# Performance work log

Measured on AMD Instinct MI355X. Metric: run time of the kernel, lower is better.

Reference implementation:

```python
import jax, jax.numpy as jnp
from jax import lax
import numpy as np

B, S, MEL = 64, 1024, 60
H, L = 180, 4
FS = 3          # mel_smooth_filter_size (num shifted conv branches)
BLOCKS = 3      # mel_smooth_layers
G = MEL // FS   # 20 output units per grouped conv
POST, OUT = 8192, 300


def setup_inputs() -> dict:
    key = jax.random.key(0)
    ks = jax.random.split(key, 13)
    rn = lambda k, shape, s: jax.random.normal(k, shape, jnp.float32) * s
    x = jax.random.normal(ks[0], (B, S, MEL), jnp.float32)
    lens = jax.random.randint(ks[1], (B,), 1, S + 1)
    conv_w = rn(ks[2], (BLOCKS, FS, G, FS, 5), 0.2)   # per block, per shift: (O=20, I/g=3, k=5)
    conv_b = rn(ks[3], (BLOCKS, FS, G), 0.1)
    lstm_wih0 = rn(ks[4], (4 * H, MEL), 0.08)
    lstm_wih_rest = rn(ks[5], (L - 1, 4 * H, H), 0.08)
    lstm_whh = rn(ks[6], (L, 4 * H, H), 0.08)
    lstm_bih = rn(ks[7], (L, 4 * H), 0.05)
    lstm_bhh = rn(ks[8], (L, 4 * H), 0.05)
    post_w = rn(ks[9], (POST, H), 0.05)
    post_b = rn(ks[10], (POST,), 0.05)
    up_w = rn(ks[11], (OUT, POST), 0.02)
    up_b = rn(ks[12], (OUT,), 0.02)
    return dict(x=x, lens=lens, conv_w=conv_w, conv_b=conv_b,
                lstm_wih0=lstm_wih0, lstm_wih_rest=lstm_wih_rest, lstm_whh=lstm_whh,
                lstm_bih=lstm_bih, lstm_bhh=lstm_bhh,
                post_w=post_w, post_b=post_b, up_w=up_w, up_b=up_b)


def _mel_block(xc, w, b):
    # xc: (B, MEL, S); w: (FS, G, FS, 5); b: (FS, G)
    zrow = jnp.zeros_like(xc[:, :1])
    xs = []
    for i in range(FS - 2):  # shift channels down by i+1
        n = i + 1
        xs.append(jnp.concatenate([jnp.zeros_like(xc[:, :n]), xc[:, :-n]], axis=1))
    xs.append(xc)
    xs.append(jnp.concatenate([xc[:, 1:], zrow], axis=1))  # shift channels up by 1
    outs = []
    for j in range(FS):
        o = lax.conv_general_dilated(xs[j], w[j], (1,), [(2, 2)],
                                     dimension_numbers=('NCH', 'OIH', 'NCH'),
                                     feature_group_count=G)
        outs.append(o + b[j][None, :, None])  # (B, G, S)
    # interleave: out channel FS*i + j = outs[j][:, i]
    return jnp.stack(outs, axis=2).reshape(xc.shape[0], MEL, xc.shape[2])


def _lstm_layer(h_in, wih, whh, bih, bhh):
    # h_in: (B, T, I). Torch gate order: i, f, g, o.
    pre = jnp.einsum('bti,gi->btg', h_in, wih) + (bih + bhh)  # (B, T, 4H)
    pre = pre.transpose(1, 0, 2)  # (T, B, 4H)
    h0 = jnp.zeros((h_in.shape[0], H), h_in.dtype)

    def step(carry, p):
        hh, cc = carry
        gates = p + hh @ whh.T
        i, f, g, o = jnp.split(gates, 4, axis=-1)
        cc = jax.nn.sigmoid(f) * cc + jax.nn.sigmoid(i) * jnp.tanh(g)
        hh = jax.nn.sigmoid(o) * jnp.tanh(cc)
        return (hh, cc), hh

    _, outs = lax.scan(step, (h0, h0), pre)
    return outs.transpose(1, 0, 2)  # (B, T, H)


def reference(x, lens, conv_w, conv_b, lstm_wih0, lstm_wih_rest, lstm_whh,
              lstm_bih, lstm_bhh, post_w, post_b, up_w, up_b):
    xc = x.transpose(0, 2, 1)  # (B, MEL, S)
    for blk in range(BLOCKS):
        shortcut = xc
        xc = _mel_block(xc, conv_w[blk], conv_b[blk]) + shortcut  # resid activation = Identity
    h = xc.transpose(0, 2, 1)  # (B, S, MEL)
    for l in range(L):
        wih = lstm_wih0 if l == 0 else lstm_wih_rest[l - 1]
        h = _lstm_layer(h, wih, lstm_whh[l], lstm_bih[l], lstm_bhh[l])
    idx = jnp.clip(lens - 1, 0, S - 1)
    last = h[jnp.arange(h.shape[0]), idx]  # (B, H)
    post = jax.nn.leaky_relu(last @ post_w.T + post_b, 0.01)  # LeakyReLU default slope
    return post @ up_w.T + up_b  # (B, OUT)
```

## Files before the change

### kernel.cpp

```cpp
#include <hip/hip_runtime.h>
#include <hip/hip_fp16.h>

#define BB 64
#define SS 1024
#define MEL 60
#define HH 180
#define G4 720
#define KP 192
#define NL 4
#define NPOST 8192
#define NOUT 300
#define NOUTP 320
#define KSPL 16
#define TT 128
#define CH 64
#define NCH (SS / CH)
#define KPAIR 96

#if defined(__has_builtin)
#if __has_builtin(__builtin_amdgcn_fdot2)
#define HAVE_FDOT2 1
#endif
#endif
#ifndef HAVE_FDOT2
#define HAVE_FDOT2 0
#endif

__device__ __forceinline__ float fdot2u(unsigned int w, unsigned int h, float acc) {
#if HAVE_FDOT2
    typedef _Float16 h2_t __attribute__((ext_vector_type(2)));
    union U { unsigned int u; h2_t v; };
    U a, b;
    a.u = w; b.u = h;
    return __builtin_amdgcn_fdot2(a.v, b.v, acc, false);
#else
    __half2 aw = *reinterpret_cast<const __half2*>(&w);
    __half2 ah = *reinterpret_cast<const __half2*>(&h);
    acc += __half2float(__low2half(aw)) * __half2float(__low2half(ah));
    acc += __half2float(__high2half(aw)) * __half2float(__high2half(ah));
    return acc;
#endif
}

__global__ void prep_w16(const float* __restrict__ whh, unsigned short* __restrict__ w16) {
    int idx = blockIdx.x * blockDim.x + threadIdx.x;
    int total = NL * KP * G4;
    if (idx >= total) return;
    int l = idx / (KP * G4);
    int r = idx % (KP * G4);
    int k8 = r / (G4 * 8);
    int r2 = r % (G4 * 8);
    int g = r2 / 8, jj = r2 % 8;
    int k = 8 * k8 + jj;
    float v = (k < HH) ? whh[((size_t)l * G4 + g) * HH + k] : 0.f;
    w16[idx] = __half_as_ushort(__float2half(v));
}

__global__ void prep_wih16(const float* __restrict__ wih0, const float* __restrict__ wih_rest,
                           unsigned int* __restrict__ w) {
    int idx = blockIdx.x * blockDim.x + threadIdx.x;
    int total = NL * G4 * KPAIR;
    if (idx >= total) return;
    int l = idx / (G4 * KPAIR);
    int r = idx % (G4 * KPAIR);
    int g = r / KPAIR, kp = r % KPAIR;
    int K = (l == 0) ? MEL : HH;
    const float* src = (l == 0) ? (wih0 + (size_t)g * MEL)
                                : (wih_rest + ((size_t)(l - 1) * G4 + g) * HH);
    float a = 0.f, b = 0.f;
    if (2 * kp < K) { a = src[2 * kp]; b = src[2 * kp + 1]; }
    __half2 h2 = __floats2half2_rn(a, b);
    w[idx] = *(unsigned int*)&h2;
}

__global__ void prep_bsum(const float* __restrict__ bih, const float* __restrict__ bhh,
                          float* __restrict__ bsum) {
    int idx = blockIdx.x * blockDim.x + threadIdx.x;
    if (idx >= NL * G4) return;
    bsum[idx] = bih[idx] + bhh[idx];
}

template <typename TIN>
__global__ __launch_bounds__(256) void mel_block(const TIN* __restrict__ in,
                                                 __half* __restrict__ out,
                                                 const float* __restrict__ w,
                                                 const float* __restrict__ bias) {
    __shared__ float xt[TT + 4][MEL];
    __shared__ float ws[900];
    __shared__ float bs[MEL];
    int bb = blockIdx.x;
    int t0 = blockIdx.y * TT;
    int tid = threadIdx.x;
    const TIN* inb = in + (size_t)bb * SS * MEL;
    for (int idx = tid; idx < (TT + 4) * MEL; idx += 256) {
        int tt = idx / MEL, ch = idx % MEL;
        int t = t0 + tt - 2;
        xt[tt][ch] = (t >= 0 && t < SS) ? (float)inb[(size_t)t * MEL + ch] : 0.f;
    }
    for (int idx = tid; idx < 900; idx += 256) ws[idx] = w[idx];
    if (tid < MEL) bs[tid] = bias[(tid % 3) * 20 + tid / 3];
    __syncthreads();
    for (int idx = tid; idx < TT * MEL; idx += 256) {
        int tt = idx / MEL, ch = idx % MEL;
        int i = ch / 3, j = ch % 3;
        int qb = 3 * i + (j - 1);
        float acc = bs[ch];
        #pragma unroll
        for (int c = 0; c < 3; ++c) {
            int q = qb + c;
            if (q >= 0 && q < MEL) {
                const float* wp = ws + ((j * 20 + i) * 3 + c) * 5;
                #pragma unroll
                for (int k = 0; k < 5; ++k) acc += xt[tt + k][q] * wp[k];
            }
        }
        out[(size_t)bb * SS * MEL + (size_t)(t0 + tt) * MEL + ch] =
            __float2half(acc + xt[tt + 2][ch]);
    }
}

struct GemmArgs {
    const __half* A[16];
    const unsigned int* W[16];
    const float* bs[16];
    __half* C[16];
    size_t cbs[16];
    int K[16];
    int KT[16];
    int t0[16];
};

__global__ __launch_bounds__(256) void gemm_pre(GemmArgs ga) {
    int j = blockIdx.z;
    int K = ga.K[j], KT = ga.KT[j];
    const __half* Ab = ga.A[j] + ((size_t)blockIdx.x * SS + ga.t0[j]) * K;
    __half* Cb = ga.C[j] + (size_t)blockIdx.x * ga.cbs[j];
    const unsigned int* Wj = ga.W[j];
    const float* bsum = ga.bs[j];
    __shared__ unsigned int A16[8][72];
    __shared__ unsigned int W16[8][72];
    int n0 = blockIdx.y * 64;
    int tid = threadIdx.x;
    int tx = tid & 15, ty = tid >> 4;
    int kpl = tid & 7, mg = tid >> 3;
    float acc[4][4];
    #pragma unroll
    for (int i = 0; i < 4; ++i)
        #pragma unroll
        for (int jn = 0; jn < 4; ++jn) acc[i][jn] = 0.f;

    for (int kt = 0; kt < KT; ++kt) {
        int kp = kt * 8 + kpl;
        #pragma unroll
        for (int r = 0; r < 2; ++r) {
            int m = mg + 32 * r;
            unsigned int av = 0u;
            if (2 * kp < K) av = *(const unsigned int*)(Ab + (size_t)m * K + 2 * kp);
            A16[kpl][m] = av;
            int g = n0 + m;
            W16[kpl][m] = (g < G4) ? Wj[(size_t)g * KPAIR + kp] : 0u;
        }
        __syncthreads();
        #pragma unroll
        for (int k = 0; k < 8; ++k) {
            unsigned int a[4], b[4];
            #pragma unroll
            for (int i = 0; i < 4; ++i) a[i] = A16[k][ty + (i << 4)];
            #pragma unroll
            for (int jn = 0; jn < 4; ++jn) b[jn] = W16[k][(tx << 2) + jn];
            #pragma unroll
            for (int i = 0; i < 4; ++i)
                #pragma unroll
                for (int jn = 0; jn < 4; ++jn) acc[i][jn] = fdot2u(b[jn], a[i], acc[i][jn]);
        }
        __syncthreads();
    }
    int g0 = n0 + (tx << 2);
    if (g0 < G4) {
        #pragma unroll
        for (int i = 0; i < 4; ++i) {
            int m = ty + (i << 4);
            __half2 p0 = __floats2half2_rn(acc[i][0] + bsum[g0], acc[i][1] + bsum[g0 + 1]);
            __half2 p1 = __floats2half2_rn(acc[i][2] + bsum[g0 + 2], acc[i][3] + bsum[g0 + 3]);
            *(__half2*)(Cb + (size_t)m * G4 + g0) = p0;
            *(__half2*)(Cb + (size_t)m * G4 + g0 + 2) = p1;
        }
    }
}

struct ScanArgs {
    const __half* pre[NL];
    size_t pbs[NL];
    const unsigned short* w4[NL];
    __half* hout[NL];
    float* hst[NL];
    float* cst[NL];
    int t0[NL];
};

__global__ __launch_bounds__(768) __attribute__((amdgpu_waves_per_eu(3, 3)))
void lstm_scan(ScanArgs sa) {
    int j = blockIdx.x / BB, b = blockIdx.x % BB;
    int tid = threadIdx.x;
    int t0 = sa.t0[j];
    const __half* preb = sa.pre[j] + (size_t)b * sa.pbs[j];
    const uint4* w4 = (const uint4*)sa.w4[j];
    __half* houtb = sa.hout[j] + ((size_t)b * SS + (size_t)t0) * HH;
    float* hstb = sa.hst[j] + b * HH;
    float* cstb = sa.cst[j] + b * HH;

    __shared__ __align__(16) unsigned short hs[KP];
    __shared__ float gates[G4];

    uint4 wreg[24];
    if (tid < G4) {
        #pragma unroll
        for (int k8 = 0; k8 < 24; ++k8) wreg[k8] = w4[k8 * G4 + tid];
    }
    #pragma unroll
    for (int k8 = 0; k8 < 24; ++k8)
        asm volatile("" : "+v"(wreg[k8].x), "+v"(wreg[k8].y), "+v"(wreg[k8].z), "+v"(wreg[k8].w));

    float c = 0.f;
    if (tid < KP) {
        float hv = 0.f;
        if (t0 > 0 && tid < HH) { hv = hstb[tid]; c = cstb[tid]; }
        hs[tid] = __half_as_ushort(__float2half(hv));
    }
    __syncthreads();

    float pre_cur = (tid < G4) ? __half2float(preb[tid]) : 0.f;
    float hlast = 0.f;
    for (int t = 0; t < CH; ++t) {
        float pre_nxt = 0.f;
        if (tid < G4 && t + 1 < CH) pre_nxt = __half2float(preb[(size_t)(t + 1) * G4 + tid]);
        if (tid < G4) {
            float acc = pre_cur;
            const uint4* hv4 = (const uint4*)hs;
            #pragma unroll
            for (int k8 = 0; k8 < 24; ++k8) {
                uint4 h8 = hv4[k8];
                uint4 w8 = wreg[k8];
                acc = fdot2u(w8.x, h8.x, acc);
                acc = fdot2u(w8.y, h8.y, acc);
                acc = fdot2u(w8.z, h8.z, acc);
                acc = fdot2u(w8.w, h8.w, acc);
            }
            gates[tid] = acc;
        }
        __syncthreads();
        if (tid < HH) {
            float gi = gates[tid], gf = gates[HH + tid];
            float gg = gates[2 * HH + tid], go = gates[3 * HH + tid];
            float si = 1.f / (1.f + __expf(-gi));
            float sf = 1.f / (1.f + __expf(-gf));
            float so = 1.f / (1.f + __expf(-go));
            float tg = 1.f - 2.f / (__expf(2.f * gg) + 1.f);
            c = sf * c + si * tg;
            float hn = so * (1.f - 2.f / (__expf(2.f * c) + 1.f));
            __half hh = __float2half(hn);
            hs[tid] = __half_as_ushort(hh);
            hlast = __half2float(hh);
            houtb[(size_t)t * HH + tid] = hh;
        }
        __syncthreads();
        pre_cur = pre_nxt;
    }
    if (tid < HH) { hstb[tid] = hlast; cstb[tid] = c; }
}

__global__ void gather_last(const __half* __restrict__ hfin, const int* __restrict__ lens,
                            float* __restrict__ last) {
    int idx = blockIdx.x * blockDim.x + threadIdx.x;
    if (idx >= BB * HH) return;
    int b = idx / HH, d = idx % HH;
    int t = lens[b] - 1;
    t = t < 0 ? 0 : (t > SS - 1 ? SS - 1 : t);
    last[idx] = __half2float(hfin[((size_t)b * SS + t) * HH + d]);
}

__global__ __launch_bounds__(256) void post_gemm(const float* __restrict__ A,
                                                 const float* __restrict__ Bw,
                                                 const float* __restrict__ pb,
                                                 float* __restrict__ Cb) {
    __shared__ float As[16][68];
    __shared__ float Bs[16][68];
    int n0 = blockIdx.x * 64;
    int tid = threadIdx.x;
    int kk = tid & 15, q = tid >> 4;
    int tx = tid & 15, ty = tid >> 4;
    float acc[4][4];
    #pragma unroll
    for (int i = 0; i < 4; ++i)
        #pragma unroll
        for (int jj = 0; jj < 4; ++jj) acc[i][jj] = 0.f;
    for (int kt = 0; kt < 12; ++kt) {
        int kidx = kt * 16 + kk;
        bool kval = kidx < HH;
        #pragma unroll
        for (int r = 0; r < 4; ++r)
            As[kk][q + (r << 4)] = kval ? A[(size_t)(q + (r << 4)) * HH + kidx] : 0.f;
        #pragma unroll
        for (int r = 0; r < 4; ++r)
            Bs[kk][q + (r << 4)] = kval ? Bw[(size_t)(n0 + q + (r << 4)) * HH + kidx] : 0.f;
        __syncthreads();
        #pragma unroll
        for (int k = 0; k < 16; ++k) {
            float a[4], bv[4];
            #pragma unroll
            for (int i = 0; i < 4; ++i) a[i] = As[k][ty + (i << 4)];
            #pragma unroll
            for (int jj = 0; jj < 4; ++jj) bv[jj] = Bs[k][(tx << 2) + jj];
            #pragma unroll
            for (int i = 0; i < 4; ++i)
                #pragma unroll
                for (int jj = 0; jj < 4; ++jj) acc[i][jj] = fmaf(a[i], bv[jj], acc[i][jj]);
        }
        __syncthreads();
    }
    #pragma unroll
    for (int i = 0; i < 4; ++i) {
        int m = ty + (i << 4);
        #pragma unroll
        for (int jj = 0; jj < 4; ++jj) {
            int g = n0 + (tx << 2) + jj;
            float v = acc[i][jj] + pb[g];
            Cb[(size_t)m * NPOST + g] = v > 0.f ? v : 0.01f * v;
        }
    }
}

__global__ __launch_bounds__(256) void up_gemm(const float* __restrict__ A,
                                               const float* __restrict__ Bw,
                                               float* __restrict__ part) {
    __shared__ float As[16][68];
    __shared__ float Bs[16][68];
    int n0 = blockIdx.x * 64;
    int k0 = blockIdx.y * (NPOST / KSPL);
    float* Pb = part + (size_t)blockIdx.y * BB * NOUTP;
    int tid = threadIdx.x;
    int kk = tid & 15, q = tid >> 4;
    int tx = tid & 15, ty = tid >> 4;
    float acc[4][4];
    #pragma unroll
    for (int i = 0; i < 4; ++i)
        #pragma unroll
        for (int jj = 0; jj < 4; ++jj) acc[i][jj] = 0.f;
    for (int kt = 0; kt < (NPOST / KSPL) / 16; ++kt) {
        int kidx = k0 + kt * 16 + kk;
        #pragma unroll
        for (int r = 0; r < 4; ++r)
            As[kk][q + (r << 4)] = A[(size_t)(q + (r << 4)) * NPOST + kidx];
        #pragma unroll
        for (int r = 0; r < 4; ++r) {
            int g = n0 + q + (r << 4);
            Bs[kk][q + (r << 4)] = (g < NOUT) ? Bw[(size_t)g * NPOST + kidx] : 0.f;
        }
        __syncthreads();
        #pragma unroll
        for (int k = 0; k < 16; ++k) {
            float a[4], bv[4];
            #pragma unroll
            for (int i = 0; i < 4; ++i) a[i] = As[k][ty + (i << 4)];
            #pragma unroll
            for (int jj = 0; jj < 4; ++jj) bv[jj] = Bs[k][(tx << 2) + jj];
            #pragma unroll
            for (int i = 0; i < 4; ++i)
                #pragma unroll
                for (int jj = 0; jj < 4; ++jj) acc[i][jj] = fmaf(a[i], bv[jj], acc[i][jj]);
        }
        __syncthreads();
    }
    #pragma unroll
    for (int i = 0; i < 4; ++i) {
        int m = ty + (i << 4);
        #pragma unroll
        for (int jj = 0; jj < 4; ++jj) {
            int g = n0 + (tx << 2) + jj;
            Pb[(size_t)m * NOUTP + g] = acc[i][jj];
        }
    }
}

__global__ void up_reduce(const float* __restrict__ part, const float* __restrict__ ub,
                          float* __restrict__ out) {
    int idx = blockIdx.x * blockDim.x + threadIdx.x;
    if (idx >= BB * NOUT) return;
    int b = idx / NOUT, o = idx % NOUT;
    float acc = ub[o];
    #pragma unroll
    for (int ks = 0; ks < KSPL; ++ks)
        acc += part[((size_t)ks * BB + b) * NOUTP + o];
    out[(size_t)b * NOUT + o] = acc;
}

extern "C" void kernel_launch(void* const* d_in, const int* in_sizes, int n_in,
                              void* d_out, int out_size, void* d_ws, size_t ws_size,
                              hipStream_t stream) {
    const float* x        = (const float*)d_in[0];
    const int*   lens     = (const int*)d_in[1];
    const float* conv_w   = (const float*)d_in[2];
    const float* conv_b   = (const float*)d_in[3];
    const float* wih0     = (const float*)d_in[4];
    const float* wih_rest = (const float*)d_in[5];
    const float* whh      = (const float*)d_in[6];
    const float* bih      = (const float*)d_in[7];
    const float* bhh      = (const float*)d_in[8];
    const float* post_w   = (const float*)d_in[9];
    const float* post_b   = (const float*)d_in[10];
    const float* up_w     = (const float*)d_in[11];
    const float* up_b     = (const float*)d_in[12];
    float* out = (float*)d_out;
    (void)in_sizes; (void)n_in; (void)out_size;

    auto pad = [](size_t v) { return (v + 255) & ~(size_t)255; };
    const size_t szMel   = (size_t)BB * SS * MEL * 2;
    const size_t szH     = (size_t)BB * SS * HH * 2;
    const size_t szPre0  = (size_t)BB * SS * G4 * 2;
    const size_t szSlot  = (size_t)BB * CH * G4 * 2;
    const size_t szW16   = (size_t)NL * KP * G4 * 2;
    const size_t szWih   = (size_t)NL * G4 * KPAIR * 4;
    const size_t szBsum  = (size_t)NL * G4 * 4;
    const size_t szState = (size_t)NL * BB * HH * 4;
    const size_t szLast  = (size_t)BB * HH * 4;
    const size_t szPost  = (size_t)BB * NPOST * 4;
    const size_t szPart  = (size_t)KSPL * BB * NOUTP * 4;

    size_t commonSmall = pad(szW16) + pad(szWih) + pad(szBsum) + 2 * pad(szState) +
                         pad(szLast) + pad(szPost) + pad(szPart) + 4096;
    size_t need1 = pad(szMel) + 4 * pad(szH) + pad(szPre0) + 3 * pad(szSlot) + commonSmall;
    size_t need2 = pad(szMel) + 4 * pad(szH) + 4 * pad(szSlot) + commonSmall;
    int tier = (ws_size >= need1) ? 1 : ((ws_size >= need2) ? 2 : 3);

    char* wsp = (char*)d_ws;
    size_t off = 0;
    auto alloc = [&](size_t bytes) -> void* {
        void* p = wsp + off;
        off = (off + bytes + 255) & ~(size_t)255;
        return p;
    };

    __half* melF = (__half*)alloc(szMel);
    __half* hbuf[NL];
    if (tier <= 2) {
        for (int l = 0; l < NL; ++l) hbuf[l] = (__half*)alloc(szH);
    } else {
        __half* p0 = (__half*)alloc(szH);
        __half* p1 = (__half*)alloc(szH);
        hbuf[0] = p0; hbuf[1] = p1; hbuf[2] = p0; hbuf[3] = p1;
    }
    __half* pre0 = nullptr;
    __half* slot[NL] = {nullptr, nullptr, nullptr, nullptr};
    if (tier == 1) {
        pre0 = (__half*)alloc(szPre0);
        for (int l = 1; l < NL; ++l) slot[l] = (__half*)alloc(szSlot);
    } else if (tier == 2) {
        for (int l = 0; l < NL; ++l) slot[l] = (__half*)alloc(szSlot);
    } else {
        slot[0] = (__half*)alloc(szSlot);
        for (int l = 1; l < NL; ++l) slot[l] = slot[0];
    }
    unsigned short* w16 = (unsigned short*)alloc(szW16);
    unsigned int* wih16 = (unsigned int*)alloc(szWih);
    float* bsum  = (float*)alloc(szBsum);
    float* hstates = (float*)alloc(szState);
    float* cstates = (float*)alloc(szState);
    float* lastb = (float*)alloc(szLast);
    float* postb = (float*)alloc(szPost);
    float* partb = (float*)alloc(szPart);

    prep_w16<<<(NL * KP * G4 + 255) / 256, 256, 0, stream>>>(whh, w16);
    prep_wih16<<<(NL * G4 * KPAIR + 255) / 256, 256, 0, stream>>>(wih0, wih_rest, wih16);
    prep_bsum<<<(NL * G4 + 255) / 256, 256, 0, stream>>>(bih, bhh, bsum);

    {
        __half* m0 = hbuf[0];
        __half* m1 = (__half*)((char*)hbuf[0] + pad(szMel));
        mel_block<float><<<dim3(BB, SS / TT), 256, 0, stream>>>(x, m0, conv_w + 0 * 900, conv_b + 0 * 60);
        mel_block<__half><<<dim3(BB, SS / TT), 256, 0, stream>>>(m0, m1, conv_w + 1 * 900, conv_b + 1 * 60);
        mel_block<__half><<<dim3(BB, SS / TT), 256, 0, stream>>>(m1, melF, conv_w + 2 * 900, conv_b + 2 * 60);
    }

    auto setGemmJob = [&](GemmArgs& ga, int nj, int l, int c) {
        ga.A[nj]  = (l == 0) ? melF : hbuf[l - 1];
        ga.K[nj]  = (l == 0) ? MEL : HH;
        ga.KT[nj] = (l == 0) ? 4 : 12;
        ga.W[nj]  = wih16 + (size_t)l * G4 * KPAIR;
        ga.bs[nj] = bsum + l * G4;
        if (tier == 1 && l == 0) {
            ga.C[nj] = pre0 + (size_t)c * CH * G4;
            ga.cbs[nj] = (size_t)SS * G4;
        } else {
            ga.C[nj] = slot[l];
            ga.cbs[nj] = (size_t)CH * G4;
        }
        ga.t0[nj] = c * CH;
    };
    auto setScanJob = [&](ScanArgs& sa, int nj, int l, int c) {
        if (tier == 1 && l == 0) {
            sa.pre[nj] = pre0 + (size_t)c * CH * G4;
            sa.pbs[nj] = (size_t)SS * G4;
        } else {
            sa.pre[nj] = slot[l];
            sa.pbs[nj] = (size_t)CH * G4;
        }
        sa.w4[nj]   = w16 + (size_t)l * KP * G4;
        sa.hout[nj] = hbuf[l];
        sa.hst[nj]  = hstates + (size_t)l * BB * HH;
        sa.cst[nj]  = cstates + (size_t)l * BB * HH;
        sa.t0[nj]   = c * CH;
    };

    if (tier <= 2) {
        if (tier == 1) {
            GemmArgs ga{};
            for (int c = 0; c < NCH; ++c) setGemmJob(ga, c, 0, c);
            gemm_pre<<<dim3(BB, 12, NCH), 256, 0, stream>>>(ga);
        }
        int lmin = (tier == 1) ? 1 : 0;
        for (int w = 0; w < NCH + NL - 1; ++w) {
            GemmArgs ga{};
            int njg = 0;
            for (int l = lmin; l < NL; ++l) {
                int c = w - l;
                if (c < 0 || c >= NCH) continue;
                setGemmJob(ga, njg++, l, c);
            }
            if (njg) gemm_pre<<<dim3(BB, 12, njg), 256, 0, stream>>>(ga);
            ScanArgs sa{};
            int njs = 0;
            for (int l = 0; l < NL; ++l) {
                int c = w - l;
                if (c < 0 || c >= NCH) continue;
                setScanJob(sa, njs++, l, c);
            }
            if (njs) lstm_scan<<<dim3(njs * BB), 768, 0, stream>>>(sa);
        }
    } else {
        for (int l = 0; l < NL; ++l) {
            for (int c = 0; c < NCH; ++c) {
                GemmArgs ga{}; ScanArgs sa{};
                setGemmJob(ga, 0, l, c);
                gemm_pre<<<dim3(BB, 12, 1), 256, 0, stream>>>(ga);
                setScanJob(sa, 0, l, c);
                lstm_scan<<<dim3(BB), 768, 0, stream>>>(sa);
            }
        }
    }

    gather_last<<<(BB * HH + 255) / 256, 256, 0, stream>>>(hbuf[NL - 1], lens, lastb);
    post_gemm<<<NPOST / 64, 256, 0, stream>>>(lastb, post_w, post_b, postb);
    up_gemm<<<dim3(NOUTP / 64, KSPL), 256, 0, stream>>>(postb, up_w, partb);
    up_reduce<<<(BB * NOUT + 255) / 256, 256, 0, stream>>>(partb, up_b, out);
}
```

Measured before the change: 2.539 ms.

## Use MFMA matrix instructions for LSTM recurrent matvec in scan kernel

Replaces the per-thread fdot2 dot-product chain in the LSTM recurrence with 16x16x32 f16 MFMA instructions. The recurrent weights are repacked into MFMA B-fragment layout and held in registers across 12 waves. The hidden state is broadcast as the A operand, and only row 0 of each result is stored. The pre-activation add moves into the gate nonlinearity stage. This shortens the serial dependent chain per step, at the cost of computing 15 redundant rows per MFMA.

```diff
diff --git a/kernel.cpp b/kernel.cpp
--- a/kernel.cpp
+++ b/kernel.cpp
@@ -6,6 +6,9 @@
 #define MEL 60
 #define HH 180
 #define G4 720
+#define G4P 768
+#define NCG 48
+#define NKS 6
 #define KP 192
 #define NL 4
 #define NPOST 8192
@@ -16,6 +19,9 @@
 #define CH 64
 #define NCH (SS / CH)
 #define KPAIR 96
+
+typedef _Float16 f16x8 __attribute__((ext_vector_type(8)));
+typedef float f32x4 __attribute__((ext_vector_type(4)));
 
 #if defined(__has_builtin)
 #if __has_builtin(__builtin_amdgcn_fdot2)
@@ -42,18 +48,31 @@
 #endif
 }
 
-__global__ void prep_w16(const float* __restrict__ whh, unsigned short* __restrict__ w16) {
+union WU { uint4 u; f16x8 f; };
+
+__global__ void prep_wmf(const float* __restrict__ whh, uint4* __restrict__ wmf) {
     int idx = blockIdx.x * blockDim.x + threadIdx.x;
-    int total = NL * KP * G4;
+    int total = NL * NCG * NKS * 64;
     if (idx >= total) return;
-    int l = idx / (KP * G4);
-    int r = idx % (KP * G4);
-    int k8 = r / (G4 * 8);
-    int r2 = r % (G4 * 8);
-    int g = r2 / 8, jj = r2 % 8;
-    int k = 8 * k8 + jj;
-    float v = (k < HH) ? whh[((size_t)l * G4 + g) * HH + k] : 0.f;
-    w16[idx] = __half_as_ushort(__float2half(v));
+    int l = idx / (NCG * NKS * 64);
+    int r = idx % (NCG * NKS * 64);
+    int cg = r / (NKS * 64);
+    int r2 = r % (NKS * 64);
+    int ks = r2 / 64, lane = r2 % 64;
+    int col = cg * 16 + (lane & 15);
+    unsigned short v[8];
+    #pragma unroll
+    for (int j = 0; j < 8; ++j) {
+        int k = ks * 32 + ((lane >> 4) << 3) + j;
+        float f = (k < HH && col < G4) ? whh[((size_t)l * G4 + col) * HH + k] : 0.f;
+        v[j] = __half_as_ushort(__float2half(f));
+    }
+    uint4 u;
+    u.x = (unsigned)v[0] | ((unsigned)v[1] << 16);
+    u.y = (unsigned)v[2] | ((unsigned)v[3] << 16);
+    u.z = (unsigned)v[4] | ((unsigned)v[5] << 16);
+    u.w = (unsigned)v[6] | ((unsigned)v[7] << 16);
+    wmf[idx] = u;
 }
 
 __global__ void prep_wih16(const float* __restrict__ wih0, const float* __restrict__ wih_rest,
@@ -191,7 +210,7 @@
 struct ScanArgs {
     const __half* pre[NL];
     size_t pbs[NL];
-    const unsigned short* w4[NL];
+    const uint4* wmf[NL];
     __half* hout[NL];
     float* hst[NL];
     float* cst[NL];
@@ -202,26 +221,28 @@
 void lstm_scan(ScanArgs sa) {
     int j = blockIdx.x / BB, b = blockIdx.x % BB;
     int tid = threadIdx.x;
+    int wv = tid >> 6, lane = tid & 63;
     int t0 = sa.t0[j];
     const __half* preb = sa.pre[j] + (size_t)b * sa.pbs[j];
-    const uint4* w4 = (const uint4*)sa.w4[j];
+    const uint4* wmf = sa.wmf[j];
     __half* houtb = sa.hout[j] + ((size_t)b * SS + (size_t)t0) * HH;
     float* hstb = sa.hst[j] + b * HH;
     float* cstb = sa.cst[j] + b * HH;
 
     __shared__ __align__(16) unsigned short hs[KP];
-    __shared__ float gates[G4];
-
-    uint4 wreg[24];
-    if (tid < G4) {
-        #pragma unroll
-        for (int k8 = 0; k8 < 24; ++k8) wreg[k8] = w4[k8 * G4 + tid];
-    }
-    #pragma unroll
-    for (int k8 = 0; k8 < 24; ++k8)
-        asm volatile("" : "+v"(wreg[k8].x), "+v"(wreg[k8].y), "+v"(wreg[k8].z), "+v"(wreg[k8].w));
-
-    float c = 0.f;
+    __shared__ float gates[G4P];
+
+    uint4 wfr[24];
+    #pragma unroll
+    for (int q = 0; q < 4; ++q)
+        #pragma unroll
+        for (int ks = 0; ks < NKS; ++ks)
+            wfr[q * NKS + ks] = wmf[(((size_t)(wv * 4 + q)) * NKS + ks) * 64 + lane];
+    #pragma unroll
+    for (int r = 0; r < 24; ++r)
+        asm volatile("" : "+v"(wfr[r].x), "+v"(wfr[r].y), "+v"(wfr[r].z), "+v"(wfr[r].w));
+
+    float c = 0.f, hlast = 0.f;
     if (tid < KP) {
         float hv = 0.f;
         if (t0 > 0 && tid < HH) { hv = hstb[tid]; c = cstb[tid]; }
@@ -229,29 +250,54 @@
     }
     __syncthreads();
 
-    float pre_cur = (tid < G4) ? __half2float(preb[tid]) : 0.f;
-    float hlast = 0.f;
+    float pc0 = 0.f, pc1 = 0.f, pc2 = 0.f, pc3 = 0.f;
+    if (tid < HH) {
+        pc0 = __half2float(preb[tid]);
+        pc1 = __half2float(preb[HH + tid]);
+        pc2 = __half2float(preb[2 * HH + tid]);
+        pc3 = __half2float(preb[3 * HH + tid]);
+    }
+
+    int hoff = (lane >> 4) << 4;
     for (int t = 0; t < CH; ++t) {
-        float pre_nxt = 0.f;
-        if (tid < G4 && t + 1 < CH) pre_nxt = __half2float(preb[(size_t)(t + 1) * G4 + tid]);
-        if (tid < G4) {
-            float acc = pre_cur;
-            const uint4* hv4 = (const uint4*)hs;
-            #pragma unroll
-            for (int k8 = 0; k8 < 24; ++k8) {
-                uint4 h8 = hv4[k8];
-                uint4 w8 = wreg[k8];
-                acc = fdot2u(w8.x, h8.x, acc);
-                acc = fdot2u(w8.y, h8.y, acc);
-                acc = fdot2u(w8.z, h8.z, acc);
-                acc = fdot2u(w8.w, h8.w, acc);
-            }
-            gates[tid] = acc;
+        float pn0 = 0.f, pn1 = 0.f, pn2 = 0.f, pn3 = 0.f;
+        if (tid < HH && t + 1 < CH) {
+            const __half* pp = preb + (size_t)(t + 1) * G4 + tid;
+            pn0 = __half2float(pp[0]);
+            pn1 = __half2float(pp[HH]);
+            pn2 = __half2float(pp[2 * HH]);
+            pn3 = __half2float(pp[3 * HH]);
+        }
+        f16x8 hf[NKS];
+        #pragma unroll
+        for (int ks = 0; ks < NKS; ++ks) {
+            WU hu;
+            hu.u = *(const uint4*)((const char*)hs + ks * 64 + hoff);
+            hf[ks] = hu.f;
+        }
+        f32x4 acc0 = {0.f, 0.f, 0.f, 0.f}, acc1 = acc0, acc2 = acc0, acc3 = acc0;
+        #pragma unroll
+        for (int ks = 0; ks < NKS; ++ks) {
+            WU w0, w1, w2, w3;
+            w0.u = wfr[0 * NKS + ks]; w1.u = wfr[1 * NKS + ks];
+            w2.u = wfr[2 * NKS + ks]; w3.u = wfr[3 * NKS + ks];
+            acc0 = __builtin_amdgcn_mfma_f32_16x16x32_f16(hf[ks], w0.f, acc0, 0, 0, 0);
+            acc1 = __builtin_amdgcn_mfma_f32_16x16x32_f16(hf[ks], w1.f, acc1, 0, 0, 0);
+            acc2 = __builtin_amdgcn_mfma_f32_16x16x32_f16(hf[ks], w2.f, acc2, 0, 0, 0);
+            acc3 = __builtin_amdgcn_mfma_f32_16x16x32_f16(hf[ks], w3.f, acc3, 0, 0, 0);
+        }
+        if (lane < 16) {
+            gates[(wv * 4 + 0) * 16 + lane] = acc0[0];
+            gates[(wv * 4 + 1) * 16 + lane] = acc1[0];
+            gates[(wv * 4 + 2) * 16 + lane] = acc2[0];
+            gates[(wv * 4 + 3) * 16 + lane] = acc3[0];
         }
         __syncthreads();
         if (tid < HH) {
-            float gi = gates[tid], gf = gates[HH + tid];
-            float gg = gates[2 * HH + tid], go = gates[3 * HH + tid];
+            float gi = gates[tid] + pc0;
+            float gf = gates[HH + tid] + pc1;
+            float gg = gates[2 * HH + tid] + pc2;
+            float go = gates[3 * HH + tid] + pc3;
             float si = 1.f / (1.f + __expf(-gi));
             float sf = 1.f / (1.f + __expf(-gf));
             float so = 1.f / (1.f + __expf(-go));
@@ -264,7 +310,7 @@
             houtb[(size_t)t * HH + tid] = hh;
         }
         __syncthreads();
-        pre_cur = pre_nxt;
+        pc0 = pn0; pc1 = pn1; pc2 = pn2; pc3 = pn3;
     }
     if (tid < HH) { hstb[tid] = hlast; cstb[tid] = c; }
 }
@@ -418,7 +464,7 @@
     const size_t szH     = (size_t)BB * SS * HH * 2;
     const size_t szPre0  = (size_t)BB * SS * G4 * 2;
     const size_t szSlot  = (size_t)BB * CH * G4 * 2;
-    const size_t szW16   = (size_t)NL * KP * G4 * 2;
+    const size_t szWmf   = (size_t)NL * NCG * NKS * 64 * 16;
     const size_t szWih   = (size_t)NL * G4 * KPAIR * 4;
     const size_t szBsum  = (size_t)NL * G4 * 4;
     const size_t szState = (size_t)NL * BB * HH * 4;
@@ -426,7 +472,7 @@
     const size_t szPost  = (size_t)BB * NPOST * 4;
     const size_t szPart  = (size_t)KSPL * BB * NOUTP * 4;
 
-    size_t commonSmall = pad(szW16) + pad(szWih) + pad(szBsum) + 2 * pad(szState) +
+    size_t commonSmall = pad(szWmf) + pad(szWih) + pad(szBsum) + 2 * pad(szState) +
                          pad(szLast) + pad(szPost) + pad(szPart) + 4096;
     size_t need1 = pad(szMel) + 4 * pad(szH) + pad(szPre0) + 3 * pad(szSlot) + commonSmall;
     size_t need2 = pad(szMel) + 4 * pad(szH) + 4 * pad(szSlot) + commonSmall;
@@ -460,7 +506,7 @@
         slot[0] = (__half*)alloc(szSlot);
         for (int l = 1; l < NL; ++l) slot[l] = slot[0];
     }
-    unsigned short* w16 = (unsigned short*)alloc(szW16);
+    uint4* wmf = (uint4*)alloc(szWmf);
     unsigned int* wih16 = (unsigned int*)alloc(szWih);
     float* bsum  = (float*)alloc(szBsum);
     float* hstates = (float*)alloc(szState);
@@ -469,7 +515,7 @@
     float* postb = (float*)alloc(szPost);
     float* partb = (float*)alloc(szPart);
 
-    prep_w16<<<(NL * KP * G4 + 255) / 256, 256, 0, stream>>>(whh, w16);
+    prep_wmf<<<(NL * NCG * NKS * 64 + 255) / 256, 256, 0, stream>>>(whh, wmf);
     prep_wih16<<<(NL * G4 * KPAIR + 255) / 256, 256, 0, stream>>>(wih0, wih_rest, wih16);
     prep_bsum<<<(NL * G4 + 255) / 256, 256, 0, stream>>>(bih, bhh, bsum);
 
@@ -504,7 +550,7 @@
             sa.pre[nj] = slot[l];
             sa.pbs[nj] = (size_t)CH * G4;
         }
-        sa.w4[nj]   = w16 + (size_t)l * KP * G4;
+        sa.wmf[nj]  = wmf + (size_t)l * NCG * NKS * 64;
         sa.hout[nj] = hbuf[l];
         sa.hst[nj]  = hstates + (size_t)l * BB * HH;
         sa.cst[nj]  = cstates + (size_t)l * BB * HH;
```

Result: faster. 2.183 ms (-14.0%).
